# Optimization experiments

Measured on AMD Instinct MI355X. Metric: run time of the kernel, lower is better.

Reference implementation:

```python
import jax, jax.numpy as jnp
import numpy as np

BATCH, IN_F, OUT_F = 8192, 2048, 2048
LN2 = float(np.log(2.0))


def setup_inputs() -> dict:
    key = jax.random.key(0)
    kx, kw = jax.random.split(key)
    x = jax.random.normal(kx, (BATCH, IN_F), dtype=jnp.float32)
    # kaiming_uniform_(a=sqrt(5)) on (OUT_F, IN_F+1): U(-1/sqrt(fan_in), 1/sqrt(fan_in))
    bound = 1.0 / np.sqrt(IN_F + 1)
    W = jax.random.uniform(kw, (OUT_F, IN_F + 1), dtype=jnp.float32,
                           minval=-bound, maxval=bound)
    W = W.at[:, -1].set(0.0)  # bias column initialized to 0
    return {"x": x, "W": W}


def reference(x, W):
    # UniversalKANNode forward, node_type='add', use_bias=True,
    # function = lshifted_softplus: f(x, w) = w * (softplus(x) - ln2)
    # Append bias ones column: (B, IN_F+1)
    xb = jnp.concatenate([x, jnp.ones((x.shape[0], 1), dtype=x.dtype)], axis=-1)
    phi = jax.nn.softplus(xb) - jnp.asarray(LN2, dtype=x.dtype)  # (B, IN_F+1)
    # sum over input dim of W[o,i] * phi[b,i]  ==  GEMM
    return jnp.einsum("bi,oi->bo", phi, W)  # (B, OUT_F)
```

## Files before the change

kernel.cpp:

```cpp
#include <hip/hip_runtime.h>

#define M_DIM 8192
#define N_DIM 2048
#define K_DIM 2048
#define LN2F 0.69314718055994530942f
#define LOG2EF 1.44269504088896340736f
#define BIAS_PHI 0.62009741f

typedef _Float16 f16x8 __attribute__((ext_vector_type(8)));
typedef float f32x4 __attribute__((ext_vector_type(4)));

__device__ __forceinline__ float softplus_m_ln2(float v) {
    float t = v * LOG2EF;
    float e = __builtin_amdgcn_exp2f(t);
    float r = (__builtin_amdgcn_logf(1.0f + e) - 1.0f) * LN2F;
    return t < 24.0f ? r : v - LN2F;
}

__global__ __launch_bounds__(256) void prep_kernel(const float* __restrict__ x,
                                                   const float* __restrict__ W,
                                                   _Float16* __restrict__ phi,
                                                   _Float16* __restrict__ Wh,
                                                   float* __restrict__ bias) {
    if (blockIdx.x < 8192) {
        size_t i = ((size_t)blockIdx.x * blockDim.x + threadIdx.x) * 8;
        float4 v0 = *(const float4*)(x + i);
        float4 v1 = *(const float4*)(x + i + 4);
        union { _Float16 h[8]; uint4 u; } pk;
        pk.h[0] = (_Float16)softplus_m_ln2(v0.x);
        pk.h[1] = (_Float16)softplus_m_ln2(v0.y);
        pk.h[2] = (_Float16)softplus_m_ln2(v0.z);
        pk.h[3] = (_Float16)softplus_m_ln2(v0.w);
        pk.h[4] = (_Float16)softplus_m_ln2(v1.x);
        pk.h[5] = (_Float16)softplus_m_ln2(v1.y);
        pk.h[6] = (_Float16)softplus_m_ln2(v1.z);
        pk.h[7] = (_Float16)softplus_m_ln2(v1.w);
        *(uint4*)(phi + i) = pk.u;
    } else {
        const int o = blockIdx.x - 8192;
        const float* row = W + (size_t)o * (K_DIM + 1) + threadIdx.x * 8;
        union { _Float16 h[8]; uint4 u; } pk;
#pragma unroll
        for (int j = 0; j < 8; ++j)
            pk.h[j] = (_Float16)row[j];
        *(uint4*)(Wh + (size_t)o * K_DIM + threadIdx.x * 8) = pk.u;
        if (threadIdx.x == 0)
            bias[o] = W[(size_t)o * (K_DIM + 1) + K_DIM] * BIAS_PHI;
    }
}

__global__ __launch_bounds__(256) void kan_gemm(const _Float16* __restrict__ A,
                                                const _Float16* __restrict__ B,
                                                const float* __restrict__ bias,
                                                float* __restrict__ C) {
    __shared__ __align__(16) _Float16 sA[128 * 64];
    __shared__ __align__(16) _Float16 sB[128 * 64];

    const int tid  = threadIdx.x;
    const int lane = tid & 63;
    const int wv   = tid >> 6;

    const size_t Arow0 = (size_t)blockIdx.x * 128;
    const size_t Brow0 = (size_t)blockIdx.y * 128;

    const int r8 = lane >> 3;
    const int pc = lane & 7;
    const int lc = pc ^ r8;

    const _Float16* gA = A + (Arow0 + wv * 32 + r8) * (size_t)K_DIM + lc * 8;
    const _Float16* gB = B + (Brow0 + wv * 32 + r8) * (size_t)K_DIM + lc * 8;
    _Float16* sAw = &sA[wv * 32 * 64];
    _Float16* sBw = &sB[wv * 32 * 64];

    const int wr = (wv >> 1) * 64;
    const int wc = (wv & 1) * 64;
    const int lr   = lane & 15;
    const int kph0 = (((lane >> 4)) ^ (lr & 7)) * 8;

    f32x4 acc[4][4];
#pragma unroll
    for (int i = 0; i < 4; ++i)
#pragma unroll
        for (int j = 0; j < 4; ++j)
            acc[i][j] = (f32x4){0.0f, 0.0f, 0.0f, 0.0f};

    for (int k0 = 0; k0 < K_DIM; k0 += 64) {
        __syncthreads();
#pragma unroll
        for (int j = 0; j < 4; ++j) {
            __builtin_amdgcn_global_load_lds(
                (const __attribute__((address_space(1))) void*)(gA + k0 + (size_t)j * 8 * K_DIM),
                (__attribute__((address_space(3))) void*)(sAw + j * 8 * 64), 16, 0, 0);
            __builtin_amdgcn_global_load_lds(
                (const __attribute__((address_space(1))) void*)(gB + k0 + (size_t)j * 8 * K_DIM),
                (__attribute__((address_space(3))) void*)(sBw + j * 8 * 64), 16, 0, 0);
        }
        __syncthreads();

#pragma unroll
        for (int kc = 0; kc < 2; ++kc) {
            const int ko = kph0 ^ (kc * 32);
            f16x8 af[4], bfr[4];
#pragma unroll
            for (int mi = 0; mi < 4; ++mi)
                af[mi] = *(const f16x8*)&sA[(wr + mi * 16 + lr) * 64 + ko];
#pragma unroll
            for (int ni = 0; ni < 4; ++ni)
                bfr[ni] = *(const f16x8*)&sB[(wc + ni * 16 + lr) * 64 + ko];

#pragma unroll
            for (int mi = 0; mi < 4; ++mi)
#pragma unroll
                for (int ni = 0; ni < 4; ++ni)
                    acc[mi][ni] = __builtin_amdgcn_mfma_f32_16x16x32_f16(
                        af[mi], bfr[ni], acc[mi][ni], 0, 0, 0);
        }
    }

    const int crow = (lane >> 4) * 4;
    float bsv[4];
#pragma unroll
    for (int ni = 0; ni < 4; ++ni)
        bsv[ni] = bias[Brow0 + wc + ni * 16 + lr];

#pragma unroll
    for (int mi = 0; mi < 4; ++mi) {
#pragma unroll
        for (int r = 0; r < 4; ++r) {
            float* cp = C + (Arow0 + wr + mi * 16 + crow + r) * (size_t)N_DIM
                        + Brow0 + wc + lr;
#pragma unroll
            for (int ni = 0; ni < 4; ++ni)
                cp[ni * 16] = acc[mi][ni][r] + bsv[ni];
        }
    }
}

extern "C" void kernel_launch(void* const* d_in, const int* in_sizes, int n_in,
                              void* d_out, int out_size, void* d_ws, size_t ws_size,
                              hipStream_t stream) {
    const float* x = (const float*)d_in[0];
    const float* W = (const float*)d_in[1];
    float* out = (float*)d_out;

    char* ws = (char*)d_ws;
    _Float16* phi = (_Float16*)ws;
    _Float16* Wh  = (_Float16*)(ws + (size_t)M_DIM * K_DIM * sizeof(_Float16));
    float* bias   = (float*)(ws + (size_t)M_DIM * K_DIM * sizeof(_Float16)
                                + (size_t)N_DIM * K_DIM * sizeof(_Float16));

    prep_kernel<<<8192 + 2048, 256, 0, stream>>>(x, W, phi, Wh, bias);
    dim3 grid(M_DIM / 128, N_DIM / 128);
    kan_gemm<<<grid, 256, 0, stream>>>(phi, Wh, bias, out);
}
```

Baseline: 194.7 us.

## Load B fragments directly from global into registers, bypassing LDS

The B (weight) tile is no longer staged through shared memory. Each lane loads its MFMA B fragments straight from global memory into registers for both k-halves. This halves LDS traffic and LDS footprint, which could raise occupancy. In exchange, each B element is now read from global/L2 by both waves that share a column half rather than once per block, and the register-load latency sits inside the barrier-bound loop.

Result: slower. 264.1 us (+35.7%).

```diff
diff --git a/kernel.cpp b/kernel.cpp
--- a/kernel.cpp
+++ b/kernel.cpp
@@ -54,7 +54,6 @@
                                                 const float* __restrict__ bias,
                                                 float* __restrict__ C) {
     __shared__ __align__(16) _Float16 sA[128 * 64];
-    __shared__ __align__(16) _Float16 sB[128 * 64];
 
     const int tid  = threadIdx.x;
     const int lane = tid & 63;
@@ -64,18 +63,19 @@
     const size_t Brow0 = (size_t)blockIdx.y * 128;
 
     const int r8 = lane >> 3;
-    const int pc = lane & 7;
-    const int lc = pc ^ r8;
-
+    const int lc = (lane & 7) ^ r8;
     const _Float16* gA = A + (Arow0 + wv * 32 + r8) * (size_t)K_DIM + lc * 8;
-    const _Float16* gB = B + (Brow0 + wv * 32 + r8) * (size_t)K_DIM + lc * 8;
     _Float16* sAw = &sA[wv * 32 * 64];
-    _Float16* sBw = &sB[wv * 32 * 64];
 
     const int wr = (wv >> 1) * 64;
     const int wc = (wv & 1) * 64;
     const int lr   = lane & 15;
-    const int kph0 = (((lane >> 4)) ^ (lr & 7)) * 8;
+    const int kph0 = ((lane >> 4) ^ (lr & 7)) * 8;
+
+    const _Float16* pB[4];
+#pragma unroll
+    for (int ni = 0; ni < 4; ++ni)
+        pB[ni] = B + (Brow0 + wc + ni * 16 + lr) * (size_t)K_DIM + (lane >> 4) * 8;
 
     f32x4 acc[4][4];
 #pragma unroll
@@ -85,36 +85,44 @@
             acc[i][j] = (f32x4){0.0f, 0.0f, 0.0f, 0.0f};
 
     for (int k0 = 0; k0 < K_DIM; k0 += 64) {
+        f16x8 b0[4], b1[4];
+#pragma unroll
+        for (int ni = 0; ni < 4; ++ni)
+            b0[ni] = *(const f16x8*)(pB[ni] + k0);
+
         __syncthreads();
 #pragma unroll
-        for (int j = 0; j < 4; ++j) {
+        for (int j = 0; j < 4; ++j)
             __builtin_amdgcn_global_load_lds(
                 (const __attribute__((address_space(1))) void*)(gA + k0 + (size_t)j * 8 * K_DIM),
                 (__attribute__((address_space(3))) void*)(sAw + j * 8 * 64), 16, 0, 0);
-            __builtin_amdgcn_global_load_lds(
-                (const __attribute__((address_space(1))) void*)(gB + k0 + (size_t)j * 8 * K_DIM),
-                (__attribute__((address_space(3))) void*)(sBw + j * 8 * 64), 16, 0, 0);
-        }
+
+#pragma unroll
+        for (int ni = 0; ni < 4; ++ni)
+            b1[ni] = *(const f16x8*)(pB[ni] + k0 + 32);
+
         __syncthreads();
 
+        f16x8 af[4];
 #pragma unroll
-        for (int kc = 0; kc < 2; ++kc) {
-            const int ko = kph0 ^ (kc * 32);
-            f16x8 af[4], bfr[4];
+        for (int mi = 0; mi < 4; ++mi)
+            af[mi] = *(const f16x8*)&sA[(wr + mi * 16 + lr) * 64 + kph0];
 #pragma unroll
-            for (int mi = 0; mi < 4; ++mi)
-                af[mi] = *(const f16x8*)&sA[(wr + mi * 16 + lr) * 64 + ko];
+        for (int mi = 0; mi < 4; ++mi)
 #pragma unroll
             for (int ni = 0; ni < 4; ++ni)
-                bfr[ni] = *(const f16x8*)&sB[(wc + ni * 16 + lr) * 64 + ko];
+                acc[mi][ni] = __builtin_amdgcn_mfma_f32_16x16x32_f16(
+                    af[mi], b0[ni], acc[mi][ni], 0, 0, 0);
 
 #pragma unroll
-            for (int mi = 0; mi < 4; ++mi)
+        for (int mi = 0; mi < 4; ++mi)
+            af[mi] = *(const f16x8*)&sA[(wr + mi * 16 + lr) * 64 + (kph0 ^ 32)];
 #pragma unroll
-                for (int ni = 0; ni < 4; ++ni)
-                    acc[mi][ni] = __builtin_amdgcn_mfma_f32_16x16x32_f16(
-                        af[mi], bfr[ni], acc[mi][ni], 0, 0, 0);
-        }
+        for (int mi = 0; mi < 4; ++mi)
+#pragma unroll
+            for (int ni = 0; ni < 4; ++ni)
+                acc[mi][ni] = __builtin_amdgcn_mfma_f32_16x16x32_f16(
+                    af[mi], b1[ni], acc[mi][ni], 0, 0, 0);
     }
 
     const int crow = (lane >> 4) * 4;
```
